# Kernel tuning notes

Hardware: AMD Instinct MI355X
Metric: run time of the kernel (lower is better)

Reference implementation:

```python
import jax, jax.numpy as jnp
import numpy as np

# Model dims (match init_kwargs)
H = 1024            # hidden_size
I = 2048            # intermediate_size (per expert)
NH = 16             # num_heads
HD = H // NH        # head_dim = 64
E = 8               # num_experts
TOPK = 2
MAX_SEQ = 2048
EPS = 1e-6
NEG = -1e9


def precompute_freqs_cis(dim, max_seq_len, theta=10000.0):
    # Faithful to source: cat([cos, sin], dim=-1) -> shape [S, dim]
    pos = np.arange(max_seq_len, dtype=np.float32)
    freqs = np.arange(0, dim, 2, dtype=np.float32) / dim
    inv_freq = 1.0 / (theta ** freqs)
    f = np.einsum('i,j->ij', pos, inv_freq)
    return jnp.asarray(np.concatenate([np.cos(f), np.sin(f)], axis=-1), dtype=jnp.float32)


def setup_inputs() -> dict:
    key = jax.random.key(0)
    ks = jax.random.split(key, 12)
    B, S = 2, 1024
    s = lambda fan: 1.0 / np.sqrt(fan)
    inp = {
        'x': jax.random.normal(ks[0], (B, S, H), dtype=jnp.float32),
        'attn_norm_w': jnp.ones((H,), dtype=jnp.float32),
        'ffn_norm_w': jnp.ones((H,), dtype=jnp.float32),
        'wq': jax.random.normal(ks[1], (H, H), dtype=jnp.float32) * s(H),
        'wk': jax.random.normal(ks[2], (H, H), dtype=jnp.float32) * s(H),
        'wv': jax.random.normal(ks[3], (H, H), dtype=jnp.float32) * s(H),
        'wo': jax.random.normal(ks[4], (H, H), dtype=jnp.float32) * s(H),
        'router_w': jax.random.normal(ks[5], (H, E), dtype=jnp.float32) * s(H),
        'w1': jax.random.normal(ks[6], (E, H, I), dtype=jnp.float32) * s(H),
        'w3': jax.random.normal(ks[7], (E, H, I), dtype=jnp.float32) * s(H),
        'w2': jax.random.normal(ks[8], (E, I, H), dtype=jnp.float32) * s(I),
        'freqs_cis': precompute_freqs_cis(HD, MAX_SEQ),
    }
    return inp


def rmsnorm(x, w):
    rms = jnp.sqrt(jnp.mean(x * x, axis=-1, keepdims=True) + EPS)
    return w * (x / rms)


def apply_rope(x, freqs_cis):
    # x: [B, S, NH, HD]; faithful to source pairing (interleaved view of cat(cos,sin))
    B, S, nh, hd = x.shape
    xr = x.reshape(B, S, nh, hd // 2, 2)
    fr = freqs_cis[:S].reshape(1, S, 1, hd // 2, 2)  # position_ids = arange(S)
    a, b = xr[..., 0], xr[..., 1]
    cr, ci = fr[..., 0], fr[..., 1]
    out = jnp.stack([a * cr - b * ci, a * ci + b * cr], axis=-1)
    return out.reshape(B, S, nh, hd)


def attention(x, wq, wk, wv, wo, freqs_cis):
    B, S, _ = x.shape
    q = (x @ wq).reshape(B, S, NH, HD)
    k = (x @ wk).reshape(B, S, NH, HD)
    v = (x @ wv).reshape(B, S, NH, HD)
    q = apply_rope(q, freqs_cis)
    k = apply_rope(k, freqs_cis)
    # [B, NH, S, S]
    scores = jnp.einsum('bqhd,bkhd->bhqk', q, k) / np.sqrt(HD).astype(np.float32)
    causal = jnp.tril(jnp.ones((S, S), dtype=bool))
    scores = jnp.where(causal[None, None], scores, NEG)
    attn = jax.nn.softmax(scores, axis=-1)
    out = jnp.einsum('bhqk,bkhd->bqhd', attn, v).reshape(B, S, H)
    return out @ wo


def moe_ffn(x, router_w, w1, w2, w3):
    # x: [B, S, H] -> flatten tokens
    B, S, _ = x.shape
    xt = x.reshape(B * S, H)                      # [T, H]
    logits = xt @ router_w                        # [T, E]
    probs = jax.nn.softmax(logits, axis=-1)
    topv, topi = jax.lax.top_k(probs, TOPK)       # [T, K]
    topv = topv / jnp.sum(topv, axis=-1, keepdims=True)  # renormalize top-k weights
    # combine[t, e] = sum_k topv[t,k] * 1[topi[t,k]==e]
    combine = jnp.sum(topv[..., None] * jax.nn.one_hot(topi, E, dtype=xt.dtype), axis=1)  # [T, E]
    # SwiGLU experts, dense over experts (mathematically identical to no-drop routing)
    h1 = jnp.einsum('th,ehi->eti', xt, w1)
    h3 = jnp.einsum('th,ehi->eti', xt, w3)
    ye = jnp.einsum('eti,eih->eth', jax.nn.silu(h1) * h3, w2)  # [E, T, H]
    out = jnp.einsum('te,eth->th', combine, ye)
    return out.reshape(B, S, H)


def reference(x, attn_norm_w, ffn_norm_w, wq, wk, wv, wo, router_w, w1, w3, w2, freqs_cis):
    h = x + attention(rmsnorm(x, attn_norm_w), wq, wk, wv, wo, freqs_cis)
    out = h + moe_ffn(rmsnorm(h, ffn_norm_w), router_w, w1, w2, w3)
    return out
```

## Files before the change

kernel.cpp:

```cpp
#include <hip/hip_runtime.h>
#include <hip/hip_bf16.h>
#include <math.h>

#define HS 1024
#define IS 2048
#define NHEAD 16
#define HDIM 64
#define NEXP 8
#define BATCH 2
#define SEQ 1024
#define NTOK (BATCH*SEQ)
#define NASSIGN (NTOK*2)
#define QKVW 3072
#define PAD 72
#define MAXBLK 40

typedef short bf16x8 __attribute__((ext_vector_type(8)));
typedef float f32x4  __attribute__((ext_vector_type(4)));
typedef unsigned short u16x8 __attribute__((ext_vector_type(8)));
typedef unsigned short u16x4 __attribute__((ext_vector_type(4)));

__device__ __forceinline__ void ldsdma16(void* lds, const void* gp) {
    __builtin_amdgcn_global_load_lds(
        (const __attribute__((address_space(1))) void*)gp,
        (__attribute__((address_space(3))) void*)lds, 16, 0, 0);
}

__global__ void rmsnorm_split(const float* __restrict__ x, const float* __restrict__ w,
                              __hip_bfloat16* __restrict__ oh, __hip_bfloat16* __restrict__ ol) {
    int t = blockIdx.x;
    int tid = threadIdx.x;
    const float* row = x + (size_t)t * HS;
    float4 v4 = *(const float4*)(row + tid * 4);
    float ss = v4.x * v4.x + v4.y * v4.y + v4.z * v4.z + v4.w * v4.w;
    for (int off = 32; off > 0; off >>= 1) ss += __shfl_down(ss, off);
    __shared__ float red[4];
    if ((tid & 63) == 0) red[tid >> 6] = ss;
    __syncthreads();
    float tot = red[0] + red[1] + red[2] + red[3];
    float rr = rsqrtf(tot / (float)HS + 1e-6f);
    float4 w4 = *(const float4*)(w + tid * 4);
    float vals[4] = {w4.x * v4.x * rr, w4.y * v4.y * rr, w4.z * v4.z * rr, w4.w * v4.w * rr};
    u16x4 h4, l4;
    #pragma unroll
    for (int j = 0; j < 4; j++) {
        __hip_bfloat16 hi = __float2bfloat16(vals[j]);
        __hip_bfloat16 lo = __float2bfloat16(vals[j] - __bfloat162float(hi));
        h4[j] = *(unsigned short*)&hi;
        l4[j] = *(unsigned short*)&lo;
    }
    *(u16x4*)&oh[(size_t)t * HS + tid * 4] = h4;
    *(u16x4*)&ol[(size_t)t * HS + tid * 4] = l4;
}

__global__ void rmsnorm_dual(const float* __restrict__ x, const float* __restrict__ w,
                             float* __restrict__ outf, __hip_bfloat16* __restrict__ outb) {
    int t = blockIdx.x;
    int tid = threadIdx.x;
    const float* row = x + (size_t)t * HS;
    float4 v4 = *(const float4*)(row + tid * 4);
    float ss = v4.x * v4.x + v4.y * v4.y + v4.z * v4.z + v4.w * v4.w;
    for (int off = 32; off > 0; off >>= 1) ss += __shfl_down(ss, off);
    __shared__ float red[4];
    if ((tid & 63) == 0) red[tid >> 6] = ss;
    __syncthreads();
    float tot = red[0] + red[1] + red[2] + red[3];
    float rr = rsqrtf(tot / (float)HS + 1e-6f);
    float4 w4 = *(const float4*)(w + tid * 4);
    float4 o4 = make_float4(w4.x * v4.x * rr, w4.y * v4.y * rr, w4.z * v4.z * rr, w4.w * v4.w * rr);
    *(float4*)&outf[(size_t)t * HS + tid * 4] = o4;
    float vals[4] = {o4.x, o4.y, o4.z, o4.w};
    u16x4 b4;
    #pragma unroll
    for (int j = 0; j < 4; j++) {
        __hip_bfloat16 hi = __float2bfloat16(vals[j]);
        b4[j] = *(unsigned short*)&hi;
    }
    *(u16x4*)&outb[(size_t)t * HS + tid * 4] = b4;
}

__global__ __launch_bounds__(256) void transpose_split4(
        const float* __restrict__ wq, const float* __restrict__ wk,
        const float* __restrict__ wv, const float* __restrict__ wo,
        __hip_bfloat16* __restrict__ qkvh, __hip_bfloat16* __restrict__ qkvl,
        __hip_bfloat16* __restrict__ oh, __hip_bfloat16* __restrict__ ol) {
    int z = blockIdx.z;
    const float* src = (z == 0) ? wq : (z == 1) ? wk : (z == 2) ? wv : wo;
    __hip_bfloat16* dh = (z < 3) ? qkvh : oh;
    __hip_bfloat16* dl = (z < 3) ? qkvl : ol;
    int rowOff = (z < 3) ? z * HS : 0;
    const int R = HS, C = HS;
    __shared__ float tile[64][65];
    int c0 = blockIdx.x * 64, r0 = blockIdx.y * 64;
    int tx = threadIdx.x & 15, ty = threadIdx.x >> 4;
    #pragma unroll
    for (int p = 0; p < 4; p++) {
        int r = ty + p * 16;
        float4 v = *(const float4*)(src + (size_t)(r0 + r) * C + c0 + tx * 4);
        tile[r][tx * 4 + 0] = v.x; tile[r][tx * 4 + 1] = v.y;
        tile[r][tx * 4 + 2] = v.z; tile[r][tx * 4 + 3] = v.w;
    }
    __syncthreads();
    int cc0 = threadIdx.x >> 3, rr = (threadIdx.x & 7) * 8;
    #pragma unroll
    for (int p = 0; p < 2; p++) {
        int cc = cc0 + p * 32;
        u16x8 h8, l8;
        #pragma unroll
        for (int j = 0; j < 8; j++) {
            float v = tile[rr + j][cc];
            __hip_bfloat16 hi = __float2bfloat16(v);
            __hip_bfloat16 lo = __float2bfloat16(v - __bfloat162float(hi));
            h8[j] = *(unsigned short*)&hi;
            l8[j] = *(unsigned short*)&lo;
        }
        size_t o = (size_t)(rowOff + c0 + cc) * R + r0 + rr;
        *(u16x8*)&dh[o] = h8;
        *(u16x8*)&dl[o] = l8;
    }
}

__global__ __launch_bounds__(256) void transpose_b64(const float* __restrict__ in,
                                                     __hip_bfloat16* __restrict__ outp,
                                                     int R, int C) {
    int e = blockIdx.z;
    const float* src = in + (size_t)e * R * C;
    __hip_bfloat16* dst = outp + (size_t)e * R * C;
    __shared__ float tile[64][65];
    int c0 = blockIdx.x * 64, r0 = blockIdx.y * 64;
    int tx = threadIdx.x & 15, ty = threadIdx.x >> 4;
    #pragma unroll
    for (int p = 0; p < 4; p++) {
        int r = ty + p * 16;
        float4 v = *(const float4*)(src + (size_t)(r0 + r) * C + c0 + tx * 4);
        tile[r][tx * 4 + 0] = v.x; tile[r][tx * 4 + 1] = v.y;
        tile[r][tx * 4 + 2] = v.z; tile[r][tx * 4 + 3] = v.w;
    }
    __syncthreads();
    int cc0 = threadIdx.x >> 3, rr = (threadIdx.x & 7) * 8;
    #pragma unroll
    for (int p = 0; p < 2; p++) {
        int cc = cc0 + p * 32;
        u16x8 b8;
        #pragma unroll
        for (int j = 0; j < 8; j++) {
            __hip_bfloat16 hi = __float2bfloat16(tile[rr + j][cc]);
            b8[j] = *(unsigned short*)&hi;
        }
        *(u16x8*)&dst[(size_t)(c0 + cc) * R + r0 + rr] = b8;
    }
}

__global__ __launch_bounds__(256) void gemm_bf16x3(const __hip_bfloat16* __restrict__ Ah,
                                                   const __hip_bfloat16* __restrict__ Al,
                                                   const __hip_bfloat16* __restrict__ Bh,
                                                   const __hip_bfloat16* __restrict__ Bl,
                                                   const float* __restrict__ resid,
                                                   float* __restrict__ C,
                                                   int M, int N, int K) {
    __shared__ __align__(16) short Ahs[2][128][32];
    __shared__ __align__(16) short Als[2][128][32];
    __shared__ __align__(16) short Bhs[2][64][32];
    __shared__ __align__(16) short Bls[2][64][32];
    int bm = blockIdx.y * 128, bn = blockIdx.x * 64;
    int t = threadIdx.x;
    int wave = t >> 6, lane = t & 63;
    int wm = (wave & 1) * 64, wn = (wave >> 1) * 32;
    int fr = lane & 15, quad = lane >> 4;
    int rA = wave * 32;
    int rB = wave * 16;
    int srow = lane >> 2;
    int schunk = (lane & 3) ^ ((lane >> 3) & 3);
    const __hip_bfloat16* pAh0 = Ah + (size_t)(bm + rA + srow) * K + schunk * 8;
    const __hip_bfloat16* pAh1 = pAh0 + (size_t)16 * K;
    const __hip_bfloat16* pAl0 = Al + (size_t)(bm + rA + srow) * K + schunk * 8;
    const __hip_bfloat16* pAl1 = pAl0 + (size_t)16 * K;
    const __hip_bfloat16* pBh  = Bh + (size_t)(bn + rB + srow) * K + schunk * 8;
    const __hip_bfloat16* pBl  = Bl + (size_t)(bn + rB + srow) * K + schunk * 8;
    int ca = (quad ^ ((fr >> 1) & 3)) * 8;

    ldsdma16(&Ahs[0][rA][0],      pAh0);
    ldsdma16(&Ahs[0][rA + 16][0], pAh1);
    ldsdma16(&Als[0][rA][0],      pAl0);
    ldsdma16(&Als[0][rA + 16][0], pAl1);
    ldsdma16(&Bhs[0][rB][0],      pBh);
    ldsdma16(&Bls[0][rB][0],      pBl);

    f32x4 acc[4][2] = {};
    int NIT = K >> 5;
    for (int it = 0; it < NIT; it++) {
        int cur = it & 1;
        __syncthreads();
        if (it + 1 < NIT) {
            int k1 = (it + 1) << 5;
            int nxt = cur ^ 1;
            ldsdma16(&Ahs[nxt][rA][0],      pAh0 + k1);
            ldsdma16(&Ahs[nxt][rA + 16][0], pAh1 + k1);
            ldsdma16(&Als[nxt][rA][0],      pAl0 + k1);
            ldsdma16(&Als[nxt][rA + 16][0], pAl1 + k1);
            ldsdma16(&Bhs[nxt][rB][0],      pBh + k1);
            ldsdma16(&Bls[nxt][rB][0],      pBl + k1);
        }
        bf16x8 ah[4], bh[2], x[4];
        #pragma unroll
        for (int i = 0; i < 4; i++) ah[i] = *(const bf16x8*)&Ahs[cur][wm + i * 16 + fr][ca];
        #pragma unroll
        for (int i = 0; i < 2; i++) bh[i] = *(const bf16x8*)&Bhs[cur][wn + i * 16 + fr][ca];
        #pragma unroll
        for (int mi = 0; mi < 4; mi++)
            #pragma unroll
            for (int ni = 0; ni < 2; ni++)
                acc[mi][ni] = __builtin_amdgcn_mfma_f32_16x16x32_bf16(ah[mi], bh[ni], acc[mi][ni], 0, 0, 0);
        #pragma unroll
        for (int i = 0; i < 2; i++) x[i] = *(const bf16x8*)&Bls[cur][wn + i * 16 + fr][ca];
        #pragma unroll
        for (int mi = 0; mi < 4; mi++)
            #pragma unroll
            for (int ni = 0; ni < 2; ni++)
                acc[mi][ni] = __builtin_amdgcn_mfma_f32_16x16x32_bf16(ah[mi], x[ni], acc[mi][ni], 0, 0, 0);
        #pragma unroll
        for (int i = 0; i < 4; i++) x[i] = *(const bf16x8*)&Als[cur][wm + i * 16 + fr][ca];
        #pragma unroll
        for (int mi = 0; mi < 4; mi++)
            #pragma unroll
            for (int ni = 0; ni < 2; ni++)
                acc[mi][ni] = __builtin_amdgcn_mfma_f32_16x16x32_bf16(x[mi], bh[ni], acc[mi][ni], 0, 0, 0);
    }
    int rq = quad * 4;
    #pragma unroll
    for (int mi = 0; mi < 4; mi++) {
        #pragma unroll
        for (int r = 0; r < 4; r++) {
            size_t rowo = (size_t)(bm + wm + mi * 16 + rq + r) * N + bn + wn;
            #pragma unroll
            for (int ni = 0; ni < 2; ni++) {
                float v = acc[mi][ni][r];
                size_t o = rowo + ni * 16 + fr;
                if (resid) v += resid[o];
                C[o] = v;
            }
        }
    }
}

__global__ __launch_bounds__(256) void gemm_qkv_rope(const __hip_bfloat16* __restrict__ Ah,
                                                     const __hip_bfloat16* __restrict__ Al,
                                                     const __hip_bfloat16* __restrict__ Bh,
                                                     const __hip_bfloat16* __restrict__ Bl,
                                                     const float* __restrict__ fc,
                                                     __hip_bfloat16* __restrict__ qh, __hip_bfloat16* __restrict__ ql,
                                                     __hip_bfloat16* __restrict__ kh, __hip_bfloat16* __restrict__ kl,
                                                     __hip_bfloat16* __restrict__ vh, __hip_bfloat16* __restrict__ vl) {
    const int K = HS;
    __shared__ __align__(16) short Ahs[2][128][32];
    __shared__ __align__(16) short Als[2][128][32];
    __shared__ __align__(16) short Bhs[2][64][32];
    __shared__ __align__(16) short Bls[2][64][32];
    int bm = blockIdx.y * 128, bn = blockIdx.x * 64;
    int t = threadIdx.x;
    int wave = t >> 6, lane = t & 63;
    int wm = (wave & 1) * 64, wn = (wave >> 1) * 32;
    int fr = lane & 15, quad = lane >> 4;
    int rA = wave * 32;
    int rB = wave * 16;
    int srow = lane >> 2;
    int schunk = (lane & 3) ^ ((lane >> 3) & 3);
    const __hip_bfloat16* pAh0 = Ah + (size_t)(bm + rA + srow) * K + schunk * 8;
    const __hip_bfloat16* pAh1 = pAh0 + (size_t)16 * K;
    const __hip_bfloat16* pAl0 = Al + (size_t)(bm + rA + srow) * K + schunk * 8;
    const __hip_bfloat16* pAl1 = pAl0 + (size_t)16 * K;
    const __hip_bfloat16* pBh  = Bh + (size_t)(bn + rB + srow) * K + schunk * 8;
    const __hip_bfloat16* pBl  = Bl + (size_t)(bn + rB + srow) * K + schunk * 8;
    int ca = (quad ^ ((fr >> 1) & 3)) * 8;

    ldsdma16(&Ahs[0][rA][0],      pAh0);
    ldsdma16(&Ahs[0][rA + 16][0], pAh1);
    ldsdma16(&Als[0][rA][0],      pAl0);
    ldsdma16(&Als[0][rA + 16][0], pAl1);
    ldsdma16(&Bhs[0][rB][0],      pBh);
    ldsdma16(&Bls[0][rB][0],      pBl);

    f32x4 acc[4][2] = {};
    const int NIT = K >> 5;
    for (int it = 0; it < NIT; it++) {
        int cur = it & 1;
        __syncthreads();
        if (it + 1 < NIT) {
            int k1 = (it + 1) << 5;
            int nxt = cur ^ 1;
            ldsdma16(&Ahs[nxt][rA][0],      pAh0 + k1);
            ldsdma16(&Ahs[nxt][rA + 16][0], pAh1 + k1);
            ldsdma16(&Als[nxt][rA][0],      pAl0 + k1);
            ldsdma16(&Als[nxt][rA + 16][0], pAl1 + k1);
            ldsdma16(&Bhs[nxt][rB][0],      pBh + k1);
            ldsdma16(&Bls[nxt][rB][0],      pBl + k1);
        }
        bf16x8 ah[4], bh[2], x[4];
        #pragma unroll
        for (int i = 0; i < 4; i++) ah[i] = *(const bf16x8*)&Ahs[cur][wm + i * 16 + fr][ca];
        #pragma unroll
        for (int i = 0; i < 2; i++) bh[i] = *(const bf16x8*)&Bhs[cur][wn + i * 16 + fr][ca];
        #pragma unroll
        for (int mi = 0; mi < 4; mi++)
            #pragma unroll
            for (int ni = 0; ni < 2; ni++)
                acc[mi][ni] = __builtin_amdgcn_mfma_f32_16x16x32_bf16(ah[mi], bh[ni], acc[mi][ni], 0, 0, 0);
        #pragma unroll
        for (int i = 0; i < 2; i++) x[i] = *(const bf16x8*)&Bls[cur][wn + i * 16 + fr][ca];
        #pragma unroll
        for (int mi = 0; mi < 4; mi++)
            #pragma unroll
            for (int ni = 0; ni < 2; ni++)
                acc[mi][ni] = __builtin_amdgcn_mfma_f32_16x16x32_bf16(ah[mi], x[ni], acc[mi][ni], 0, 0, 0);
        #pragma unroll
        for (int i = 0; i < 4; i++) x[i] = *(const bf16x8*)&Als[cur][wm + i * 16 + fr][ca];
        #pragma unroll
        for (int mi = 0; mi < 4; mi++)
            #pragma unroll
            for (int ni = 0; ni < 2; ni++)
                acc[mi][ni] = __builtin_amdgcn_mfma_f32_16x16x32_bf16(x[mi], bh[ni], acc[mi][ni], 0, 0, 0);
    }
    __hip_bfloat16 *dh, *dl;
    int cbase;
    bool dorope;
    if (bn < 1024)      { dh = qh; dl = ql; cbase = bn;        dorope = true;  }
    else if (bn < 2048) { dh = kh; dl = kl; cbase = bn - 1024; dorope = true;  }
    else                { dh = vh; dl = vl; cbase = bn - 2048; dorope = false; }
    float sgn = (fr & 1) ? 1.f : -1.f;
    int rq = quad * 4;
    #pragma unroll
    for (int mi = 0; mi < 4; mi++) {
        #pragma unroll
        for (int r = 0; r < 4; r++) {
            int trow = bm + wm + mi * 16 + rq + r;
            int s = trow & (SEQ - 1);
            size_t ob = (size_t)trow * HS + cbase;
            #pragma unroll
            for (int ni = 0; ni < 2; ni++) {
                float v = acc[mi][ni][r];
                int colh = wn + ni * 16 + fr;
                float outv;
                if (dorope) {
                    float p = __shfl_xor(v, 1);
                    const float* fb = fc + (size_t)s * HDIM + (colh & ~1);
                    float cr = fb[0], ci = fb[1];
                    outv = v * cr + sgn * (p * ci);
                } else {
                    outv = v;
                }
                __hip_bfloat16 hi = __float2bfloat16(outv);
                __hip_bfloat16 lo = __float2bfloat16(outv - __bfloat162float(hi));
                dh[ob + colh] = hi;
                dl[ob + colh] = lo;
            }
        }
    }
}

__global__ __launch_bounds__(256) void attn_partial(
        const __hip_bfloat16* __restrict__ qh, const __hip_bfloat16* __restrict__ ql,
        const __hip_bfloat16* __restrict__ kh, const __hip_bfloat16* __restrict__ kl,
        const __hip_bfloat16* __restrict__ vh, const __hip_bfloat16* __restrict__ vl,
        float* __restrict__ po, float* __restrict__ pm_g, float* __restrict__ pl_g) {
    int c = blockIdx.x, qt = blockIdx.y;
    int nc = (qt + 4) >> 2;
    if (c >= nc) return;
    int bh = blockIdx.z;
    int b = bh >> 4, h = bh & 15;
    int t0 = c * 4, t1 = min(t0 + 4, qt + 1);
    int tid = threadIdx.x;
    int wave = tid >> 6, lane = tid & 63;
    int fr = lane & 15, quad = lane >> 4;
    int w16 = wave * 16;
    __shared__ __align__(16) short Qh[64][PAD], Ql[64][PAD];
    __shared__ __align__(16) short KPh[64][PAD], KPl[64][PAD];
    __shared__ __align__(16) short Vhs[64][PAD], Vls[64][PAD];
    size_t hoff = (size_t)h * HDIM;
    int sr = tid >> 2, sg = tid & 3;
    {
        const __hip_bfloat16* qp  = qh + (size_t)(b * SEQ + qt * 64 + sr) * HS + hoff;
        const __hip_bfloat16* qp2 = ql + (size_t)(b * SEQ + qt * 64 + sr) * HS + hoff;
        *(uint4*)&Qh[sr][sg * 8]       = *(const uint4*)(qp + sg * 8);
        *(uint4*)&Qh[sr][(sg + 4) * 8] = *(const uint4*)(qp + (sg + 4) * 8);
        *(uint4*)&Ql[sr][sg * 8]       = *(const uint4*)(qp2 + sg * 8);
        *(uint4*)&Ql[sr][(sg + 4) * 8] = *(const uint4*)(qp2 + (sg + 4) * 8);
    }
    f32x4 o[4] = {};
    float mrow[4], lrow[4];
    #pragma unroll
    for (int i = 0; i < 4; i++) { mrow[i] = -1e30f; lrow[i] = 0.f; }
    int key0 = (tid & 31) * 2, ds = tid >> 5;
    __syncthreads();

    for (int kt = t0; kt < t1; kt++) {
        int kbase = kt * 64;
        {
            const __hip_bfloat16* kp  = kh + (size_t)(b * SEQ + kbase + sr) * HS + hoff;
            const __hip_bfloat16* kp2 = kl + (size_t)(b * SEQ + kbase + sr) * HS + hoff;
            *(uint4*)&KPh[sr][sg * 8]       = *(const uint4*)(kp + sg * 8);
            *(uint4*)&KPh[sr][(sg + 4) * 8] = *(const uint4*)(kp + (sg + 4) * 8);
            *(uint4*)&KPl[sr][sg * 8]       = *(const uint4*)(kp2 + sg * 8);
            *(uint4*)&KPl[sr][(sg + 4) * 8] = *(const uint4*)(kp2 + (sg + 4) * 8);
        }
        {
            const __hip_bfloat16* v0 = vh + (size_t)(b * SEQ + kbase + key0) * HS + hoff + ds * 8;
            uint4 A = *(const uint4*)v0;
            uint4 Bv = *(const uint4*)(v0 + HS);
            const unsigned short* ap = (const unsigned short*)&A;
            const unsigned short* bp = (const unsigned short*)&Bv;
            #pragma unroll
            for (int j = 0; j < 8; j++)
                *(unsigned*)&Vhs[ds * 8 + j][key0] = (unsigned)ap[j] | ((unsigned)bp[j] << 16);
            const __hip_bfloat16* v2 = vl + (size_t)(b * SEQ + kbase + key0) * HS + hoff + ds * 8;
            uint4 A2 = *(const uint4*)v2;
            uint4 B2 = *(const uint4*)(v2 + HS);
            const unsigned short* ap2 = (const unsigned short*)&A2;
            const unsigned short* bp2 = (const unsigned short*)&B2;
            #pragma unroll
            for (int j = 0; j < 8; j++)
                *(unsigned*)&Vls[ds * 8 + j][key0] = (unsigned)ap2[j] | ((unsigned)bp2[j] << 16);
        }
        __syncthreads();

        f32x4 s[4] = {};
        #pragma unroll
        for (int ks = 0; ks < 2; ks++) {
            bf16x8 a_h = *(const bf16x8*)&Qh[w16 + fr][quad * 8 + ks * 32];
            bf16x8 a_l = *(const bf16x8*)&Ql[w16 + fr][quad * 8 + ks * 32];
            #pragma unroll
            for (int ni = 0; ni < 4; ni++) {
                bf16x8 b_h = *(const bf16x8*)&KPh[ni * 16 + fr][quad * 8 + ks * 32];
                bf16x8 b_l = *(const bf16x8*)&KPl[ni * 16 + fr][quad * 8 + ks * 32];
                s[ni] = __builtin_amdgcn_mfma_f32_16x16x32_bf16(a_h, b_h, s[ni], 0, 0, 0);
                s[ni] = __builtin_amdgcn_mfma_f32_16x16x32_bf16(a_h, b_l, s[ni], 0, 0, 0);
                s[ni] = __builtin_amdgcn_mfma_f32_16x16x32_bf16(a_l, b_h, s[ni], 0, 0, 0);
            }
        }
        int qg = qt * 64 + w16 + quad * 4;
        #pragma unroll
        for (int ni = 0; ni < 4; ni++) {
            int kg = kbase + ni * 16 + fr;
            #pragma unroll
            for (int r = 0; r < 4; r++)
                s[ni][r] = (kg > qg + r) ? -1e9f : s[ni][r] * 0.125f;
        }
        #pragma unroll
        for (int r = 0; r < 4; r++) {
            float mx = fmaxf(fmaxf(s[0][r], s[1][r]), fmaxf(s[2][r], s[3][r]));
            #pragma unroll
            for (int wd = 1; wd < 16; wd <<= 1) mx = fmaxf(mx, __shfl_xor(mx, wd));
            float nm = fmaxf(mrow[r], mx);
            float alpha = __expf(mrow[r] - nm);
            float rs = 0.f;
            #pragma unroll
            for (int ni = 0; ni < 4; ni++) { float e = __expf(s[ni][r] - nm); s[ni][r] = e; rs += e; }
            #pragma unroll
            for (int wd = 1; wd < 16; wd <<= 1) rs += __shfl_xor(rs, wd);
            lrow[r] = lrow[r] * alpha + rs;
            mrow[r] = nm;
            o[0][r] *= alpha; o[1][r] *= alpha; o[2][r] *= alpha; o[3][r] *= alpha;
        }
        __syncthreads();
        #pragma unroll
        for (int ni = 0; ni < 4; ni++)
            #pragma unroll
            for (int r = 0; r < 4; r++) {
                float pv = s[ni][r];
                __hip_bfloat16 hi = __float2bfloat16(pv);
                __hip_bfloat16 lo = __float2bfloat16(pv - __bfloat162float(hi));
                KPh[w16 + quad * 4 + r][ni * 16 + fr] = *(short*)&hi;
                KPl[w16 + quad * 4 + r][ni * 16 + fr] = *(short*)&lo;
            }
        #pragma unroll
        for (int ks = 0; ks < 2; ks++) {
            bf16x8 p_h = *(const bf16x8*)&KPh[w16 + fr][quad * 8 + ks * 32];
            bf16x8 p_l = *(const bf16x8*)&KPl[w16 + fr][quad * 8 + ks * 32];
            #pragma unroll
            for (int ni = 0; ni < 4; ni++) {
                bf16x8 v_h = *(const bf16x8*)&Vhs[ni * 16 + fr][quad * 8 + ks * 32];
                bf16x8 v_l = *(const bf16x8*)&Vls[ni * 16 + fr][quad * 8 + ks * 32];
                o[ni] = __builtin_amdgcn_mfma_f32_16x16x32_bf16(p_h, v_h, o[ni], 0, 0, 0);
                o[ni] = __builtin_amdgcn_mfma_f32_16x16x32_bf16(p_h, v_l, o[ni], 0, 0, 0);
                o[ni] = __builtin_amdgcn_mfma_f32_16x16x32_bf16(p_l, v_h, o[ni], 0, 0, 0);
            }
        }
        __syncthreads();
    }
    int pidx = (bh * 16 + qt) * 4 + c;
    float* pob = po + (size_t)pidx * 4096;
    #pragma unroll
    for (int ni = 0; ni < 4; ni++)
        #pragma unroll
        for (int r = 0; r < 4; r++)
            pob[(w16 + quad * 4 + r) * 64 + ni * 16 + fr] = o[ni][r];
    if (fr == 0) {
        #pragma unroll
        for (int r = 0; r < 4; r++) {
            pm_g[pidx * 64 + w16 + quad * 4 + r] = mrow[r];
            pl_g[pidx * 64 + w16 + quad * 4 + r] = lrow[r];
        }
    }
}

__global__ void attn_merge(const float* __restrict__ po, const float* __restrict__ pm,
                           const float* __restrict__ pl,
                           __hip_bfloat16* __restrict__ ch, __hip_bfloat16* __restrict__ cl) {
    int qt = blockIdx.x, h = blockIdx.y, b = blockIdx.z;
    int bh = b * 16 + h;
    int nc = (qt + 4) >> 2;
    int base = (bh * 16 + qt) * 4;
    int tid = threadIdx.x;
    int r  = tid >> 2;
    int d0 = (tid & 3) * 16;
    float mstar = -1e30f;
    for (int c = 0; c < nc; c++) mstar = fmaxf(mstar, pm[(base + c) * 64 + r]);
    float a[4];
    float lsum = 0.f;
    for (int c = 0; c < nc; c++) {
        a[c] = __expf(pm[(base + c) * 64 + r] - mstar);
        lsum += a[c] * pl[(base + c) * 64 + r];
    }
    float inv = 1.f / lsum;
    size_t crow = (size_t)(b * SEQ + qt * 64 + r) * HS + h * HDIM;
    for (int dd = 0; dd < 16; dd += 4) {
        float4 acc = make_float4(0.f, 0.f, 0.f, 0.f);
        for (int c = 0; c < nc; c++) {
            float4 v = *(const float4*)(po + (size_t)(base + c) * 4096 + r * 64 + d0 + dd);
            acc.x += a[c] * v.x; acc.y += a[c] * v.y;
            acc.z += a[c] * v.z; acc.w += a[c] * v.w;
        }
        float vs[4] = {acc.x * inv, acc.y * inv, acc.z * inv, acc.w * inv};
        #pragma unroll
        for (int j = 0; j < 4; j++) {
            __hip_bfloat16 hi = __float2bfloat16(vs[j]);
            ch[crow + d0 + dd + j] = hi;
            cl[crow + d0 + dd + j] = __float2bfloat16(vs[j] - __bfloat162float(hi));
        }
    }
}

__global__ void router_kernel(const float* __restrict__ hn, const float* __restrict__ rw,
                              int* __restrict__ cnt, int* __restrict__ topEk,
                              float* __restrict__ topW) {
    int t = blockIdx.x;
    int lane = threadIdx.x;
    float acc[NEXP];
    #pragma unroll
    for (int e = 0; e < NEXP; e++) acc[e] = 0.f;
    const float* row = hn + (size_t)t * HS;
    for (int kk = lane; kk < HS; kk += 64) {
        float xv = row[kk];
        const float* r = rw + (size_t)kk * NEXP;
        #pragma unroll
        for (int e = 0; e < NEXP; e++) acc[e] += xv * r[e];
    }
    #pragma unroll
    for (int e = 0; e < NEXP; e++)
        for (int off = 32; off > 0; off >>= 1) acc[e] += __shfl_down(acc[e], off);
    if (lane == 0) {
        float mx = acc[0];
        #pragma unroll
        for (int e = 1; e < NEXP; e++) mx = fmaxf(mx, acc[e]);
        float p[NEXP]; float s = 0.f;
        #pragma unroll
        for (int e = 0; e < NEXP; e++) { p[e] = __expf(acc[e] - mx); s += p[e]; }
        int i0 = 0;
        #pragma unroll
        for (int e = 1; e < NEXP; e++) if (p[e] > p[i0]) i0 = e;
        int i1 = (i0 == 0) ? 1 : 0;
        #pragma unroll
        for (int e = 0; e < NEXP; e++) if (e != i0 && p[e] > p[i1]) i1 = e;
        float v0 = p[i0], v1 = p[i1], sn = v0 + v1;
        topEk[2 * t]     = i0; topW[2 * t]     = v0 / sn;
        topEk[2 * t + 1] = i1; topW[2 * t + 1] = v1 / sn;
        atomicAdd(&cnt[i0], 1);
        atomicAdd(&cnt[i1], 1);
    }
}

__global__ void offsets_kernel(const int* __restrict__ cnt, int* __restrict__ off,
                               int* __restrict__ blk_e, int* __restrict__ blk_r) {
    if (threadIdx.x == 0) {
        int o = 0, n = 0;
        for (int e = 0; e < NEXP; e++) {
            off[e] = o;
            for (int bm = 0; bm < cnt[e]; bm += 128) { blk_e[n] = e; blk_r[n] = bm; n++; }
            o += cnt[e];
        }
        for (; n < MAXBLK; n++) { blk_e[n] = -1; blk_r[n] = 0; }
    }
}

__global__ void scatter_kernel(const int* __restrict__ topEk, int* __restrict__ fill,
                               const int* __restrict__ off, const float* __restrict__ topW,
                               int* __restrict__ tok_list, float* __restrict__ wA) {
    int idx = blockIdx.x * 256 + threadIdx.x;
    int e = topEk[idx];
    int slot = atomicAdd(&fill[e], 1);
    int gidx = off[e] + slot;
    tok_list[gidx] = idx >> 1;
    wA[gidx] = topW[idx];
}

__global__ __launch_bounds__(256) void moe_up_mfma(const __hip_bfloat16* __restrict__ Abf,
                                                   const __hip_bfloat16* __restrict__ B1T,
                                                   const __hip_bfloat16* __restrict__ B3T,
                                                   __hip_bfloat16* __restrict__ g,
                                                   const int* __restrict__ cnt,
                                                   const int* __restrict__ off,
                                                   const int* __restrict__ tok_list,
                                                   const int* __restrict__ blk_e,
                                                   const int* __restrict__ blk_r) {
    int e = blk_e[blockIdx.y];
    if (e < 0) return;
    int bm = blk_r[blockIdx.y];
    int ce = cnt[e], oe = off[e];
    int bn = blockIdx.x * 64;
    const __hip_bfloat16* b1 = B1T + (size_t)e * IS * HS;
    const __hip_bfloat16* b3 = B3T + (size_t)e * IS * HS;

    __shared__ __align__(16) short As[2][128][32];
    __shared__ __align__(16) short B1s[2][64][32];
    __shared__ __align__(16) short B3s[2][64][32];

    int t = threadIdx.x;
    int wave = t >> 6, lane = t & 63;
    int wm = (wave & 1) * 64, wn = (wave >> 1) * 32;
    int fr = lane & 15, quad = lane >> 4;
    int rA = wave * 32, rB = wave * 16;
    int srow = lane >> 2;
    int schunk = (lane & 3) ^ ((lane >> 3) & 3);
    int tokA0 = tok_list[oe + min(bm + rA + srow, ce - 1)];
    int tokA1 = tok_list[oe + min(bm + rA + 16 + srow, ce - 1)];
    const __hip_bfloat16* pA0 = Abf + (size_t)tokA0 * HS + schunk * 8;
    const __hip_bfloat16* pA1 = Abf + (size_t)tokA1 * HS + schunk * 8;
    const __hip_bfloat16* pB1 = b1 + (size_t)(bn + rB + srow) * HS + schunk * 8;
    const __hip_bfloat16* pB3 = b3 + (size_t)(bn + rB + srow) * HS + schunk * 8;
    int ca = (quad ^ ((fr >> 1) & 3)) * 8;

    ldsdma16(&As[0][rA][0],      pA0);
    ldsdma16(&As[0][rA + 16][0], pA1);
    ldsdma16(&B1s[0][rB][0],     pB1);
    ldsdma16(&B3s[0][rB][0],     pB3);

    f32x4 acc1[4][2] = {};
    f32x4 acc3[4][2] = {};
    const int NIT = HS >> 5;
    for (int it = 0; it < NIT; it++) {
        int cur = it & 1;
        __syncthreads();
        if (it + 1 < NIT) {
            int k1 = (it + 1) << 5;
            int nxt = cur ^ 1;
            ldsdma16(&As[nxt][rA][0],      pA0 + k1);
            ldsdma16(&As[nxt][rA + 16][0], pA1 + k1);
            ldsdma16(&B1s[nxt][rB][0],     pB1 + k1);
            ldsdma16(&B3s[nxt][rB][0],     pB3 + k1);
        }
        bf16x8 a[4], f1[2], f3[2];
        #pragma unroll
        for (int i = 0; i < 4; i++) a[i] = *(const bf16x8*)&As[cur][wm + i * 16 + fr][ca];
        #pragma unroll
        for (int i = 0; i < 2; i++) {
            f1[i] = *(const bf16x8*)&B1s[cur][wn + i * 16 + fr][ca];
            f3[i] = *(const bf16x8*)&B3s[cur][wn + i * 16 + fr][ca];
        }
        #pragma unroll
        for (int mi = 0; mi < 4; mi++)
            #pragma unroll
            for (int ni = 0; ni < 2; ni++) {
                acc1[mi][ni] = __builtin_amdgcn_mfma_f32_16x16x32_bf16(a[mi], f1[ni], acc1[mi][ni], 0, 0, 0);
                acc3[mi][ni] = __builtin_amdgcn_mfma_f32_16x16x32_bf16(a[mi], f3[ni], acc3[mi][ni], 0, 0, 0);
            }
    }
    int rq = quad * 4;
    #pragma unroll
    for (int mi = 0; mi < 4; mi++) {
        #pragma unroll
        for (int r = 0; r < 4; r++) {
            int slot = bm + wm + mi * 16 + rq + r;
            if (slot < ce) {
                size_t rowo = (size_t)(oe + slot) * IS + bn + wn;
                #pragma unroll
                for (int ni = 0; ni < 2; ni++) {
                    float x1 = acc1[mi][ni][r];
                    float x3 = acc3[mi][ni][r];
                    float sv = (x1 / (1.f + __expf(-x1))) * x3;
                    g[rowo + ni * 16 + fr] = __float2bfloat16(sv);
                }
            }
        }
    }
}

__global__ __launch_bounds__(256) void moe_down_mfma(const __hip_bfloat16* __restrict__ g,
                                                     const __hip_bfloat16* __restrict__ B2T,
                                                     float* __restrict__ out,
                                                     const int* __restrict__ cnt,
                                                     const int* __restrict__ off,
                                                     const int* __restrict__ tok_list,
                                                     const float* __restrict__ wA,
                                                     const int* __restrict__ blk_e,
                                                     const int* __restrict__ blk_r) {
    int e = blk_e[blockIdx.y];
    if (e < 0) return;
    int bm = blk_r[blockIdx.y];
    int ce = cnt[e], oe = off[e];
    int bn = blockIdx.x * 64;
    int kz = blockIdx.z * (IS / 2);
    const __hip_bfloat16* b2 = B2T + (size_t)e * HS * IS;

    __shared__ __align__(16) short As[2][128][32];
    __shared__ __align__(16) short Bs[2][64][32];

    int t = threadIdx.x;
    int wave = t >> 6, lane = t & 63;
    int wm = (wave & 1) * 64, wn = (wave >> 1) * 32;
    int fr = lane & 15, quad = lane >> 4;
    int rA = wave * 32, rB = wave * 16;
    int srow = lane >> 2;
    int schunk = (lane & 3) ^ ((lane >> 3) & 3);
    int ga0 = oe + min(bm + rA + srow, ce - 1);
    int ga1 = oe + min(bm + rA + 16 + srow, ce - 1);
    const __hip_bfloat16* pA0 = g + (size_t)ga0 * IS + kz + schunk * 8;
    const __hip_bfloat16* pA1 = g + (size_t)ga1 * IS + kz + schunk * 8;
    const __hip_bfloat16* pB  = b2 + (size_t)(bn + rB + srow) * IS + kz + schunk * 8;
    int ca = (quad ^ ((fr >> 1) & 3)) * 8;

    ldsdma16(&As[0][rA][0],      pA0);
    ldsdma16(&As[0][rA + 16][0], pA1);
    ldsdma16(&Bs[0][rB][0],      pB);

    f32x4 acc[4][2] = {};
    const int NIT = (IS / 2) >> 5;
    for (int it = 0; it < NIT; it++) {
        int cur = it & 1;
        __syncthreads();
        if (it + 1 < NIT) {
            int k1 = (it + 1) << 5;
            int nxt = cur ^ 1;
            ldsdma16(&As[nxt][rA][0],      pA0 + k1);
            ldsdma16(&As[nxt][rA + 16][0], pA1 + k1);
            ldsdma16(&Bs[nxt][rB][0],      pB + k1);
        }
        bf16x8 a[4], f[2];
        #pragma unroll
        for (int i = 0; i < 4; i++) a[i] = *(const bf16x8*)&As[cur][wm + i * 16 + fr][ca];
        #pragma unroll
        for (int i = 0; i < 2; i++) f[i] = *(const bf16x8*)&Bs[cur][wn + i * 16 + fr][ca];
        #pragma unroll
        for (int mi = 0; mi < 4; mi++)
            #pragma unroll
            for (int ni = 0; ni < 2; ni++)
                acc[mi][ni] = __builtin_amdgcn_mfma_f32_16x16x32_bf16(a[mi], f[ni], acc[mi][ni], 0, 0, 0);
    }
    int rq = quad * 4;
    #pragma unroll
    for (int mi = 0; mi < 4; mi++) {
        #pragma unroll
        for (int r = 0; r < 4; r++) {
            int slot = bm + wm + mi * 16 + rq + r;
            if (slot < ce) {
                int gidx = oe + slot;
                int tok = tok_list[gidx];
                float wgt = wA[gidx];
                size_t rowo = (size_t)tok * HS + bn + wn;
                #pragma unroll
                for (int ni = 0; ni < 2; ni++)
                    atomicAdd(out + rowo + ni * 16 + fr, wgt * acc[mi][ni][r]);
            }
        }
    }
}

extern "C" void kernel_launch(void* const* d_in, const int* in_sizes, int n_in,
                              void* d_out, int out_size, void* d_ws, size_t ws_size,
                              hipStream_t stream) {
    const float* x   = (const float*)d_in[0];
    const float* anw = (const float*)d_in[1];
    const float* fnw = (const float*)d_in[2];
    const float* wq  = (const float*)d_in[3];
    const float* wk  = (const float*)d_in[4];
    const float* wv  = (const float*)d_in[5];
    const float* wo  = (const float*)d_in[6];
    const float* rw  = (const float*)d_in[7];
    const float* w1  = (const float*)d_in[8];
    const float* w3  = (const float*)d_in[9];
    const float* w2  = (const float*)d_in[10];
    const float* fc  = (const float*)d_in[11];
    float* out = (float*)d_out;

    char* ws = (char*)d_ws;
    const size_t MB = 1024 * 1024;
    __hip_bfloat16* xn_h  = (__hip_bfloat16*)(ws + 0 * MB);
    __hip_bfloat16* xn_l  = (__hip_bfloat16*)(ws + 4 * MB);
    __hip_bfloat16* WqT_h = (__hip_bfloat16*)(ws + 32 * MB);
    __hip_bfloat16* WqT_l = (__hip_bfloat16*)(ws + 38 * MB);
    __hip_bfloat16* woT_h = (__hip_bfloat16*)(ws + 44 * MB);
    __hip_bfloat16* woT_l = (__hip_bfloat16*)(ws + 46 * MB);
    float*          po    = (float*)(ws + 48 * MB);
    float*          pm    = (float*)(ws + 82 * MB);
    float*          plb   = (float*)(ws + 83 * MB);
    __hip_bfloat16* ctx_h = (__hip_bfloat16*)(ws + 84 * MB);
    __hip_bfloat16* ctx_l = (__hip_bfloat16*)(ws + 88 * MB);
    __hip_bfloat16* qhb   = (__hip_bfloat16*)(ws + 92 * MB);
    __hip_bfloat16* qlb   = (__hip_bfloat16*)(ws + 96 * MB);
    __hip_bfloat16* khb   = (__hip_bfloat16*)(ws + 100 * MB);
    __hip_bfloat16* klb   = (__hip_bfloat16*)(ws + 104 * MB);
    __hip_bfloat16* vhb   = (__hip_bfloat16*)(ws + 108 * MB);
    __hip_bfloat16* vlb   = (__hip_bfloat16*)(ws + 112 * MB);
    float*          hn    = (float*)(ws + 0 * MB);
    __hip_bfloat16* hn_bf = (__hip_bfloat16*)(ws + 8 * MB);
    __hip_bfloat16* w1T   = (__hip_bfloat16*)(ws + 12 * MB);
    __hip_bfloat16* w3T   = (__hip_bfloat16*)(ws + 44 * MB);
    __hip_bfloat16* w2T   = (__hip_bfloat16*)(ws + 76 * MB);
    __hip_bfloat16* gact  = (__hip_bfloat16*)(ws + 108 * MB);
    int* ibase    = (int*)(ws + 124 * MB);
    int* cnt      = ibase;
    int* fill     = ibase + 8;
    int* off      = ibase + 16;
    int* blk_e    = ibase + 24;
    int* blk_r    = ibase + 64;
    int* topEk    = ibase + 128;
    int* tok_list = ibase + 128 + NASSIGN;
    float* topW   = (float*)(ibase + 128 + 2 * NASSIGN);
    float* wA     = (float*)(ibase + 128 + 3 * NASSIGN);

    transpose_split4<<<dim3(HS / 64, HS / 64, 4), 256, 0, stream>>>(
        wq, wk, wv, wo, WqT_h, WqT_l, woT_h, woT_l);
    rmsnorm_split<<<NTOK, 256, 0, stream>>>(x, anw, xn_h, xn_l);

    gemm_qkv_rope<<<dim3(QKVW / 64, NTOK / 128), 256, 0, stream>>>(
        xn_h, xn_l, WqT_h, WqT_l, fc, qhb, qlb, khb, klb, vhb, vlb);

    attn_partial<<<dim3(4, 16, 32), 256, 0, stream>>>(qhb, qlb, khb, klb, vhb, vlb, po, pm, plb);
    attn_merge<<<dim3(16, 16, 2), 256, 0, stream>>>(po, pm, plb, ctx_h, ctx_l);

    gemm_bf16x3<<<dim3(HS / 64, NTOK / 128), 256, 0, stream>>>(
        ctx_h, ctx_l, woT_h, woT_l, x, out, NTOK, HS, HS);

    rmsnorm_dual<<<NTOK, 256, 0, stream>>>(out, fnw, hn, hn_bf);
    transpose_b64<<<dim3(IS / 64, HS / 64, NEXP), 256, 0, stream>>>(w1, w1T, HS, IS);
    transpose_b64<<<dim3(IS / 64, HS / 64, NEXP), 256, 0, stream>>>(w3, w3T, HS, IS);
    transpose_b64<<<dim3(HS / 64, IS / 64, NEXP), 256, 0, stream>>>(w2, w2T, IS, HS);

    hipMemsetAsync(cnt, 0, 16 * sizeof(int), stream);
    router_kernel<<<NTOK, 64, 0, stream>>>(hn, rw, cnt, topEk, topW);
    offsets_kernel<<<1, 64, 0, stream>>>(cnt, off, blk_e, blk_r);
    scatter_kernel<<<NASSIGN / 256, 256, 0, stream>>>(topEk, fill, off, topW, tok_list, wA);

    moe_up_mfma<<<dim3(IS / 64, MAXBLK), 256, 0, stream>>>(
        hn_bf, w1T, w3T, gact, cnt, off, tok_list, blk_e, blk_r);
    moe_down_mfma<<<dim3(HS / 64, MAXBLK, 2), 256, 0, stream>>>(
        gact, w2T, out, cnt, off, tok_list, wA, blk_e, blk_r);
}
```

Before: 626.0 us.

## Fuse router into RMSNorm, merge weight transposes, replace down-proj atomics with gather

The router logits, softmax and top-2 selection now run inside the FFN RMSNorm kernel, so the fp32 normalized activations are no longer written out and read back. The three expert-weight transposes become a single launch; blocks outside each matrix's shape exit early. The counter memset is dropped and the counters are zeroed inside the first transpose kernel. The MoE down-projection now writes unweighted per-assignment results into a scratch buffer that reuses the w1T space. A new gather kernel combines them with the routing weights and the residual, replacing scattered float atomicAdds, at the cost of extra scratch traffic.

```diff
diff --git a/kernel.cpp b/kernel.cpp
--- a/kernel.cpp
+++ b/kernel.cpp
@@ -53,8 +53,11 @@
     *(u16x4*)&ol[(size_t)t * HS + tid * 4] = l4;
 }
 
-__global__ void rmsnorm_dual(const float* __restrict__ x, const float* __restrict__ w,
-                             float* __restrict__ outf, __hip_bfloat16* __restrict__ outb) {
+__global__ void rmsnorm_router(const float* __restrict__ x, const float* __restrict__ w,
+                               const float* __restrict__ rw,
+                               __hip_bfloat16* __restrict__ outb,
+                               int* __restrict__ cnt, int* __restrict__ topEk,
+                               float* __restrict__ topW) {
     int t = blockIdx.x;
     int tid = threadIdx.x;
     const float* row = x + (size_t)t * HS;
@@ -62,14 +65,13 @@
     float ss = v4.x * v4.x + v4.y * v4.y + v4.z * v4.z + v4.w * v4.w;
     for (int off = 32; off > 0; off >>= 1) ss += __shfl_down(ss, off);
     __shared__ float red[4];
+    __shared__ float lred[4][NEXP];
     if ((tid & 63) == 0) red[tid >> 6] = ss;
     __syncthreads();
     float tot = red[0] + red[1] + red[2] + red[3];
     float rr = rsqrtf(tot / (float)HS + 1e-6f);
     float4 w4 = *(const float4*)(w + tid * 4);
-    float4 o4 = make_float4(w4.x * v4.x * rr, w4.y * v4.y * rr, w4.z * v4.z * rr, w4.w * v4.w * rr);
-    *(float4*)&outf[(size_t)t * HS + tid * 4] = o4;
-    float vals[4] = {o4.x, o4.y, o4.z, o4.w};
+    float vals[4] = {w4.x * v4.x * rr, w4.y * v4.y * rr, w4.z * v4.z * rr, w4.w * v4.w * rr};
     u16x4 b4;
     #pragma unroll
     for (int j = 0; j < 4; j++) {
@@ -77,14 +79,59 @@
         b4[j] = *(unsigned short*)&hi;
     }
     *(u16x4*)&outb[(size_t)t * HS + tid * 4] = b4;
+    float acc[NEXP];
+    #pragma unroll
+    for (int e = 0; e < NEXP; e++) acc[e] = 0.f;
+    #pragma unroll
+    for (int j = 0; j < 4; j++) {
+        const float* r8 = rw + (size_t)(tid * 4 + j) * NEXP;
+        float4 ra = *(const float4*)r8;
+        float4 rb = *(const float4*)(r8 + 4);
+        float xv = vals[j];
+        acc[0] += xv * ra.x; acc[1] += xv * ra.y; acc[2] += xv * ra.z; acc[3] += xv * ra.w;
+        acc[4] += xv * rb.x; acc[5] += xv * rb.y; acc[6] += xv * rb.z; acc[7] += xv * rb.w;
+    }
+    #pragma unroll
+    for (int e = 0; e < NEXP; e++)
+        for (int off = 32; off > 0; off >>= 1) acc[e] += __shfl_down(acc[e], off);
+    if ((tid & 63) == 0) {
+        #pragma unroll
+        for (int e = 0; e < NEXP; e++) lred[tid >> 6][e] = acc[e];
+    }
+    __syncthreads();
+    if (tid == 0) {
+        float l[NEXP];
+        #pragma unroll
+        for (int e = 0; e < NEXP; e++) l[e] = lred[0][e] + lred[1][e] + lred[2][e] + lred[3][e];
+        float mx = l[0];
+        #pragma unroll
+        for (int e = 1; e < NEXP; e++) mx = fmaxf(mx, l[e]);
+        float p[NEXP]; float s = 0.f;
+        #pragma unroll
+        for (int e = 0; e < NEXP; e++) { p[e] = __expf(l[e] - mx); s += p[e]; }
+        int i0 = 0;
+        #pragma unroll
+        for (int e = 1; e < NEXP; e++) if (p[e] > p[i0]) i0 = e;
+        int i1 = (i0 == 0) ? 1 : 0;
+        #pragma unroll
+        for (int e = 0; e < NEXP; e++) if (e != i0 && p[e] > p[i1]) i1 = e;
+        float v0 = p[i0], v1 = p[i1], sn = v0 + v1;
+        topEk[2 * t]     = i0; topW[2 * t]     = v0 / sn;
+        topEk[2 * t + 1] = i1; topW[2 * t + 1] = v1 / sn;
+        atomicAdd(&cnt[i0], 1);
+        atomicAdd(&cnt[i1], 1);
+    }
 }
 
 __global__ __launch_bounds__(256) void transpose_split4(
         const float* __restrict__ wq, const float* __restrict__ wk,
         const float* __restrict__ wv, const float* __restrict__ wo,
         __hip_bfloat16* __restrict__ qkvh, __hip_bfloat16* __restrict__ qkvl,
-        __hip_bfloat16* __restrict__ oh, __hip_bfloat16* __restrict__ ol) {
+        __hip_bfloat16* __restrict__ oh, __hip_bfloat16* __restrict__ ol,
+        int* __restrict__ zbuf) {
     int z = blockIdx.z;
+    if (z == 0 && blockIdx.x == 0 && blockIdx.y == 0 && threadIdx.x < 16)
+        zbuf[threadIdx.x] = 0;
     const float* src = (z == 0) ? wq : (z == 1) ? wk : (z == 2) ? wv : wo;
     __hip_bfloat16* dh = (z < 3) ? qkvh : oh;
     __hip_bfloat16* dl = (z < 3) ? qkvl : ol;
@@ -120,14 +167,20 @@
     }
 }
 
-__global__ __launch_bounds__(256) void transpose_b64(const float* __restrict__ in,
-                                                     __hip_bfloat16* __restrict__ outp,
-                                                     int R, int C) {
-    int e = blockIdx.z;
-    const float* src = in + (size_t)e * R * C;
-    __hip_bfloat16* dst = outp + (size_t)e * R * C;
+__global__ __launch_bounds__(256) void transpose_b64_all(
+        const float* __restrict__ w1, const float* __restrict__ w3, const float* __restrict__ w2,
+        __hip_bfloat16* __restrict__ w1T, __hip_bfloat16* __restrict__ w3T,
+        __hip_bfloat16* __restrict__ w2T) {
+    int z = blockIdx.z, which = z >> 3, e = z & 7;
+    int R = (which == 2) ? IS : HS;
+    int C = (which == 2) ? HS : IS;
+    int c0 = blockIdx.x * 64, r0 = blockIdx.y * 64;
+    if (c0 >= C || r0 >= R) return;
+    const float* srcb = (which == 0) ? w1 : (which == 1) ? w3 : w2;
+    __hip_bfloat16* dstb = (which == 0) ? w1T : (which == 1) ? w3T : w2T;
+    const float* src = srcb + (size_t)e * R * C;
+    __hip_bfloat16* dst = dstb + (size_t)e * R * C;
     __shared__ float tile[64][65];
-    int c0 = blockIdx.x * 64, r0 = blockIdx.y * 64;
     int tx = threadIdx.x & 15, ty = threadIdx.x >> 4;
     #pragma unroll
     for (int p = 0; p < 4; p++) {
@@ -539,45 +592,6 @@
     }
 }
 
-__global__ void router_kernel(const float* __restrict__ hn, const float* __restrict__ rw,
-                              int* __restrict__ cnt, int* __restrict__ topEk,
-                              float* __restrict__ topW) {
-    int t = blockIdx.x;
-    int lane = threadIdx.x;
-    float acc[NEXP];
-    #pragma unroll
-    for (int e = 0; e < NEXP; e++) acc[e] = 0.f;
-    const float* row = hn + (size_t)t * HS;
-    for (int kk = lane; kk < HS; kk += 64) {
-        float xv = row[kk];
-        const float* r = rw + (size_t)kk * NEXP;
-        #pragma unroll
-        for (int e = 0; e < NEXP; e++) acc[e] += xv * r[e];
-    }
-    #pragma unroll
-    for (int e = 0; e < NEXP; e++)
-        for (int off = 32; off > 0; off >>= 1) acc[e] += __shfl_down(acc[e], off);
-    if (lane == 0) {
-        float mx = acc[0];
-        #pragma unroll
-        for (int e = 1; e < NEXP; e++) mx = fmaxf(mx, acc[e]);
-        float p[NEXP]; float s = 0.f;
-        #pragma unroll
-        for (int e = 0; e < NEXP; e++) { p[e] = __expf(acc[e] - mx); s += p[e]; }
-        int i0 = 0;
-        #pragma unroll
-        for (int e = 1; e < NEXP; e++) if (p[e] > p[i0]) i0 = e;
-        int i1 = (i0 == 0) ? 1 : 0;
-        #pragma unroll
-        for (int e = 0; e < NEXP; e++) if (e != i0 && p[e] > p[i1]) i1 = e;
-        float v0 = p[i0], v1 = p[i1], sn = v0 + v1;
-        topEk[2 * t]     = i0; topW[2 * t]     = v0 / sn;
-        topEk[2 * t + 1] = i1; topW[2 * t + 1] = v1 / sn;
-        atomicAdd(&cnt[i0], 1);
-        atomicAdd(&cnt[i1], 1);
-    }
-}
-
 __global__ void offsets_kernel(const int* __restrict__ cnt, int* __restrict__ off,
                                int* __restrict__ blk_e, int* __restrict__ blk_r) {
     if (threadIdx.x == 0) {
@@ -593,13 +607,13 @@
 
 __global__ void scatter_kernel(const int* __restrict__ topEk, int* __restrict__ fill,
                                const int* __restrict__ off, const float* __restrict__ topW,
-                               int* __restrict__ tok_list, float* __restrict__ wA) {
+                               int* __restrict__ tok_list, int* __restrict__ inv) {
     int idx = blockIdx.x * 256 + threadIdx.x;
     int e = topEk[idx];
     int slot = atomicAdd(&fill[e], 1);
     int gidx = off[e] + slot;
     tok_list[gidx] = idx >> 1;
-    wA[gidx] = topW[idx];
+    inv[idx] = gidx;
 }
 
 __global__ __launch_bounds__(256) void moe_up_mfma(const __hip_bfloat16* __restrict__ Abf,
@@ -695,11 +709,9 @@
 
 __global__ __launch_bounds__(256) void moe_down_mfma(const __hip_bfloat16* __restrict__ g,
                                                      const __hip_bfloat16* __restrict__ B2T,
-                                                     float* __restrict__ out,
+                                                     float* __restrict__ scr,
                                                      const int* __restrict__ cnt,
                                                      const int* __restrict__ off,
-                                                     const int* __restrict__ tok_list,
-                                                     const float* __restrict__ wA,
                                                      const int* __restrict__ blk_e,
                                                      const int* __restrict__ blk_r) {
     int e = blk_e[blockIdx.y];
@@ -762,15 +774,33 @@
             int slot = bm + wm + mi * 16 + rq + r;
             if (slot < ce) {
                 int gidx = oe + slot;
-                int tok = tok_list[gidx];
-                float wgt = wA[gidx];
-                size_t rowo = (size_t)tok * HS + bn + wn;
+                size_t rowo = (size_t)(blockIdx.z * NASSIGN + gidx) * HS + bn + wn;
                 #pragma unroll
                 for (int ni = 0; ni < 2; ni++)
-                    atomicAdd(out + rowo + ni * 16 + fr, wgt * acc[mi][ni][r]);
+                    scr[rowo + ni * 16 + fr] = acc[mi][ni][r];
             }
         }
     }
+}
+
+__global__ void moe_gather(const float* __restrict__ scr, const int* __restrict__ inv,
+                           const float* __restrict__ topW, float* __restrict__ out) {
+    int t = blockIdx.x;
+    int c = threadIdx.x * 4;
+    int g0 = inv[2 * t], g1 = inv[2 * t + 1];
+    float w0 = topW[2 * t], w1 = topW[2 * t + 1];
+    size_t o = (size_t)t * HS + c;
+    float4 h4 = *(const float4*)(out + o);
+    float4 a0 = *(const float4*)(scr + (size_t)g0 * HS + c);
+    float4 a1 = *(const float4*)(scr + (size_t)(NASSIGN + g0) * HS + c);
+    float4 b0 = *(const float4*)(scr + (size_t)g1 * HS + c);
+    float4 b1 = *(const float4*)(scr + (size_t)(NASSIGN + g1) * HS + c);
+    float4 r;
+    r.x = h4.x + w0 * (a0.x + a1.x) + w1 * (b0.x + b1.x);
+    r.y = h4.y + w0 * (a0.y + a1.y) + w1 * (b0.y + b1.y);
+    r.z = h4.z + w0 * (a0.z + a1.z) + w1 * (b0.z + b1.z);
+    r.w = h4.w + w0 * (a0.w + a1.w) + w1 * (b0.w + b1.w);
+    *(float4*)(out + o) = r;
 }
 
 extern "C" void kernel_launch(void* const* d_in, const int* in_sizes, int n_in,
@@ -809,9 +839,9 @@
     __hip_bfloat16* klb   = (__hip_bfloat16*)(ws + 104 * MB);
     __hip_bfloat16* vhb   = (__hip_bfloat16*)(ws + 108 * MB);
     __hip_bfloat16* vlb   = (__hip_bfloat16*)(ws + 112 * MB);
-    float*          hn    = (float*)(ws + 0 * MB);
     __hip_bfloat16* hn_bf = (__hip_bfloat16*)(ws + 8 * MB);
     __hip_bfloat16* w1T   = (__hip_bfloat16*)(ws + 12 * MB);
+    float*          dscr  = (float*)(ws + 12 * MB);
     __hip_bfloat16* w3T   = (__hip_bfloat16*)(ws + 44 * MB);
     __hip_bfloat16* w2T   = (__hip_bfloat16*)(ws + 76 * MB);
     __hip_bfloat16* gact  = (__hip_bfloat16*)(ws + 108 * MB);
@@ -824,10 +854,10 @@
     int* topEk    = ibase + 128;
     int* tok_list = ibase + 128 + NASSIGN;
     float* topW   = (float*)(ibase + 128 + 2 * NASSIGN);
-    float* wA     = (float*)(ibase + 128 + 3 * NASSIGN);
+    int*   inv    = ibase + 128 + 3 * NASSIGN;
 
     transpose_split4<<<dim3(HS / 64, HS / 64, 4), 256, 0, stream>>>(
-        wq, wk, wv, wo, WqT_h, WqT_l, woT_h, woT_l);
+        wq, wk, wv, wo, WqT_h, WqT_l, woT_h, woT_l, cnt);
     rmsnorm_split<<<NTOK, 256, 0, stream>>>(x, anw, xn_h, xn_l);
 
     gemm_qkv_rope<<<dim3(QKVW / 64, NTOK / 128), 256, 0, stream>>>(
@@ -839,18 +869,16 @@
     gemm_bf16x3<<<dim3(HS / 64, NTOK / 128), 256, 0, stream>>>(
         ctx_h, ctx_l, woT_h, woT_l, x, out, NTOK, HS, HS);
 
-    rmsnorm_dual<<<NTOK, 256, 0, stream>>>(out, fnw, hn, hn_bf);
-    transpose_b64<<<dim3(IS / 64, HS / 64, NEXP), 256, 0, stream>>>(w1, w1T, HS, IS);
-    transpose_b64<<<dim3(IS / 64, HS / 64, NEXP), 256, 0, stream>>>(w3, w3T, HS, IS);
-    transpose_b64<<<dim3(HS / 64, IS / 64, NEXP), 256, 0, stream>>>(w2, w2T, IS, HS);
-
-    hipMemsetAsync(cnt, 0, 16 * sizeof(int), stream);
-    router_kernel<<<NTOK, 64, 0, stream>>>(hn, rw, cnt, topEk, topW);
+    rmsnorm_router<<<NTOK, 256, 0, stream>>>(out, fnw, rw, hn_bf, cnt, topEk, topW);
+    transpose_b64_all<<<dim3(IS / 64, IS / 64, 24), 256, 0, stream>>>(
+        w1, w3, w2, w1T, w3T, w2T);
+
     offsets_kernel<<<1, 64, 0, stream>>>(cnt, off, blk_e, blk_r);
-    scatter_kernel<<<NASSIGN / 256, 256, 0, stream>>>(topEk, fill, off, topW, tok_list, wA);
+    scatter_kernel<<<NASSIGN / 256, 256, 0, stream>>>(topEk, fill, off, topW, tok_list, inv);
 
     moe_up_mfma<<<dim3(IS / 64, MAXBLK), 256, 0, stream>>>(
         hn_bf, w1T, w3T, gact, cnt, off, tok_list, blk_e, blk_r);
     moe_down_mfma<<<dim3(HS / 64, MAXBLK, 2), 256, 0, stream>>>(
-        gact, w2T, out, cnt, off, tok_list, wA, blk_e, blk_r);
-}
+        gact, w2T, dscr, cnt, off, blk_e, blk_r);
+    moe_gather<<<NTOK, 256, 0, stream>>>(dscr, inv, topW, out);
+}
```

New measurement: 609.5 us. -2.6%, faster.
